# Kernel tuning notes

Hardware: AMD Instinct MI355X
Metric: run time of the kernel (lower is better)

The kernel has to match this reference:

```python
import jax, jax.numpy as jnp
import numpy as np

N_NODES = 50000
N_EDGES = 640000
WIDTH = 128
K = 5
N_CONVS = 6  # 1 input + 4 hidden + 1 output ChebConv layers


def setup_inputs() -> dict:
    key = jax.random.key(0)
    k1, k2, k3, k4 = jax.random.split(key, 4)
    scale = 1.0 / np.sqrt(WIDTH)
    x = jax.random.normal(k1, (N_NODES, WIDTH), dtype=jnp.float32)
    edge_index = jax.random.randint(k2, (2, N_EDGES), 0, N_NODES, dtype=jnp.int64)
    conv_w = jax.random.normal(k3, (N_CONVS, K, WIDTH, WIDTH), dtype=jnp.float32) * scale
    conv_b = jnp.zeros((N_CONVS, WIDTH), dtype=jnp.float32)
    lin_w = jax.random.normal(k4, (WIDTH, 1), dtype=jnp.float32) * scale
    lin_b = jnp.zeros((1,), dtype=jnp.float32)
    return {"x": x, "edge_index": edge_index, "conv_w": conv_w,
            "conv_b": conv_b, "lin_w": lin_w, "lin_b": lin_b}


def _cheb_norm(edge_index):
    # PyG ChebConv with normalization='sym', lambda_max=2.0:
    # L_hat = 2/lambda_max * (I - D^-1/2 A D^-1/2) - I = -D^-1/2 A D^-1/2
    # (diagonal terms cancel), so per-edge weight = -d_i^-1/2 * d_j^-1/2.
    src, dst = edge_index[0], edge_index[1]
    ones = jnp.ones((edge_index.shape[1],), dtype=jnp.float32)
    deg = jax.ops.segment_sum(ones, dst, num_segments=N_NODES)
    d_inv_sqrt = jnp.where(deg > 0, jax.lax.rsqrt(jnp.maximum(deg, 1e-12)), 0.0)
    return -d_inv_sqrt[src] * d_inv_sqrt[dst]


def _propagate(x, src, dst, norm):
    # L_hat @ x via gather -> weight -> scatter-add
    msg = norm[:, None] * x[src]              # [E, C]
    return jax.ops.segment_sum(msg, dst, num_segments=N_NODES)


def _cheb_conv(x, W, b, src, dst, norm):
    # Chebyshev recurrence: T0=x, T1=Lx, Tk = 2*L*T(k-1) - T(k-2)
    Tx0 = x
    out = Tx0 @ W[0]
    Tx1 = _propagate(Tx0, src, dst, norm)
    out = out + Tx1 @ W[1]
    for k in range(2, K):
        Tx2 = 2.0 * _propagate(Tx1, src, dst, norm) - Tx0
        out = out + Tx2 @ W[k]
        Tx0, Tx1 = Tx1, Tx2
    return out + b


def reference(x, edge_index, conv_w, conv_b, lin_w, lin_b):
    src, dst = edge_index[0], edge_index[1]
    norm = _cheb_norm(edge_index)
    h = x
    # first 5 convs followed by ReLU (dropout is identity in eval mode)
    for l in range(N_CONVS - 1):
        h = _cheb_conv(h, conv_w[l], conv_b[l], src, dst, norm)
        h = jax.nn.relu(h)
    # final conv (no activation) + Linear(128, 1)
    h = _cheb_conv(h, conv_w[N_CONVS - 1], conv_b[N_CONVS - 1], src, dst, norm)
    return h @ lin_w + lin_b
```

## Files before the change

kernel.cpp:

```cpp
#include <hip/hip_runtime.h>


#define NN 50000
#define NE 640000
#define WID 128
#define PROP_BLOCKS 2048

typedef __attribute__((ext_vector_type(8))) short bf16x8;
typedef __attribute__((ext_vector_type(4))) float f32x4;

__device__ __forceinline__ unsigned short f2bf(float f) {
  union { float f; unsigned int u; } v; v.f = f;
  unsigned int r = v.u + 0x7FFF + ((v.u >> 16) & 1);
  return (unsigned short)(r >> 16);
}
__device__ __forceinline__ unsigned int pack2(float lo, float hi) {
  return (unsigned int)f2bf(lo) | ((unsigned int)f2bf(hi) << 16);
}
__device__ __forceinline__ float bflo(unsigned int u) {
  return __uint_as_float(u << 16);
}
__device__ __forceinline__ float bfhi(unsigned int u) {
  return __uint_as_float(u & 0xffff0000u);
}
__device__ __forceinline__ float dec_norm(unsigned int p) {
  unsigned int lo = p & 0xfffu;
  float v = -__uint_as_float(((112u + ((p >> 8) & 15u)) << 23) | ((p & 255u) << 15));
  return (lo == 0u) ? 0.f : v;
}


__global__ __launch_bounds__(256) void degree_kernel(const int* __restrict__ ei,
                                                     int* __restrict__ deg, int E) {
  int e = blockIdx.x * 256 + threadIdx.x;
  if (e < E) atomicAdd(&deg[ei[E + e]], 1);
}

__global__ __launch_bounds__(256) void scan1_kernel(const int* __restrict__ deg,
                                                    int* __restrict__ lex,
                                                    int* __restrict__ bsum,
                                                    float* __restrict__ dinv, int n) {
  __shared__ int ws[4];
  int tid = threadIdx.x, lane = tid & 63, w = tid >> 6;
  int i = blockIdx.x * 256 + tid;
  int cnt = (i < n) ? deg[i] : 0;
  if (i < n) {
    float d = (float)cnt;
    dinv[i] = d > 0.0f ? rsqrtf(d) : 0.0f;
  }
  int v = cnt;
#pragma unroll
  for (int off = 1; off < 64; off <<= 1) {
    int u = __shfl_up(v, off, 64);
    if (lane >= off) v += u;
  }
  if (lane == 63) ws[w] = v;
  __syncthreads();
  int wexcl = 0;
#pragma unroll
  for (int k = 0; k < 4; ++k) wexcl += (k < w) ? ws[k] : 0;
  if (i < n) lex[i] = wexcl + v - cnt;
  if (tid == 255) bsum[blockIdx.x] = wexcl + v;
}

__global__ __launch_bounds__(256) void scan2_kernel(const int* __restrict__ bsum,
                                                    int* __restrict__ boff,
                                                    int* __restrict__ row_end, int nb) {
  __shared__ int ws[4];
  int tid = threadIdx.x, lane = tid & 63, w = tid >> 6;
  int cnt = (tid < nb) ? bsum[tid] : 0;
  int v = cnt;
#pragma unroll
  for (int off = 1; off < 64; off <<= 1) {
    int u = __shfl_up(v, off, 64);
    if (lane >= off) v += u;
  }
  if (lane == 63) ws[w] = v;
  __syncthreads();
  int wexcl = 0;
#pragma unroll
  for (int k = 0; k < 4; ++k) wexcl += (k < w) ? ws[k] : 0;
  if (tid < nb) boff[tid] = wexcl + v - cnt;
  if (tid == 255) *row_end = wexcl + v;
}

__global__ __launch_bounds__(256) void scan3_kernel(const int* __restrict__ lex,
                                                    const int* __restrict__ boff,
                                                    int* __restrict__ row_start,
                                                    int* __restrict__ fill_ptr, int n) {
  int i = blockIdx.x * 256 + threadIdx.x;
  if (i < n) {
    int rs = lex[i] + boff[blockIdx.x];
    row_start[i] = rs;
    fill_ptr[i] = rs;
  }
}

__global__ __launch_bounds__(256) void fill_kernel(const int* __restrict__ ei,
                                                   const float* __restrict__ dinv,
                                                   int* __restrict__ fill_ptr,
                                                   unsigned int* __restrict__ csr, int E) {
  int e = blockIdx.x * 256 + threadIdx.x;
  if (e < E) {
    int s = ei[e];
    int d = ei[E + e];
    int pos = atomicAdd(&fill_ptr[d], 1);
    float mag = dinv[s] * dinv[d];
    unsigned int bits = __float_as_uint(mag);
    unsigned int pk = (unsigned int)s << 12;
    if (bits != 0u) {
      bits += 0x4000u;
      int ex = (int)((bits >> 23) & 255u) - 112;
      ex = max(0, min(15, ex));
      pk |= ((unsigned int)ex << 8) | ((bits >> 15) & 0xffu);
    }
    csr[pos] = pk;
  }
}

__global__ __launch_bounds__(256) void cvt_kernel(const float* __restrict__ x,
                                                  unsigned short* __restrict__ xo,
                                                  const float* __restrict__ w,
                                                  unsigned short* __restrict__ wt,
                                                  int nx, int nw) {
  int i = blockIdx.x * 256 + threadIdx.x;
  if (i < nx) {
    xo[i] = f2bf(x[i]);
  } else if (i < nx + nw) {
    int j = i - nx;
    int l = j / (WID * 640);
    int r = j % (WID * 640);
    int col = r / 640;
    int k = r % 640;
    int kk = k >> 7, m = k & 127;
    wt[j] = f2bf(w[(((size_t)l * 5 + kk) * WID + m) * WID + col]);
  }
}

__global__ __launch_bounds__(256) void vk_kernel(const float* __restrict__ w,
                                                 const float* __restrict__ b,
                                                 const float* __restrict__ lw,
                                                 const float* __restrict__ lb,
                                                 float* __restrict__ V,
                                                 float* __restrict__ cst) {
  int tid = threadIdx.x;
  for (int idx = tid; idx < 5 * WID; idx += 256) {
    int k = idx / WID, i = idx % WID;
    const float* wr = w + (((size_t)5 * 5 + k) * WID + i) * WID;
    float s = 0.f;
#pragma unroll 4
    for (int j = 0; j < WID; ++j) s += wr[j] * lw[j];
    V[idx] = s;
  }
  if (tid == 0) {
    float s = 0.f;
    for (int c = 0; c < WID; ++c) s += b[5 * WID + c] * lw[c];
    *cst = s + lb[0];
  }
}


__global__ __launch_bounds__(256) void prop_kernel(unsigned short* __restrict__ out,
                                                   const unsigned short* __restrict__ xin,
                                                   const unsigned short* __restrict__ sub,
                                                   float scale,
                                                   const int* __restrict__ row_start,
                                                   const unsigned int* __restrict__ csr,
                                                   int n) {
  int t = threadIdx.x & 15;
  for (int node = blockIdx.x * 16 + (threadIdx.x >> 4); node < n;
       node += PROP_BLOCKS * 16) {
    int s = row_start[node], e = row_start[node + 1];
    float a0 = 0.f, a1 = 0.f, a2 = 0.f, a3 = 0.f;
    float a4 = 0.f, a5 = 0.f, a6 = 0.f, a7 = 0.f;
    for (int base = s; base < e; base += 16) {
      int cnt = min(16, e - base);
      unsigned int ed = (t < cnt) ? csr[base + t] : 0u;
      int j = 0;
      for (; j + 4 <= cnt; j += 4) {
        unsigned int p0 = (unsigned int)__shfl((int)ed, j, 16);
        unsigned int p1 = (unsigned int)__shfl((int)ed, j + 1, 16);
        unsigned int p2 = (unsigned int)__shfl((int)ed, j + 2, 16);
        unsigned int p3 = (unsigned int)__shfl((int)ed, j + 3, 16);
        int s0 = p0 >> 12, s1 = p1 >> 12, s2 = p2 >> 12, s3 = p3 >> 12;
        float n0 = dec_norm(p0), n1 = dec_norm(p1), n2 = dec_norm(p2), n3 = dec_norm(p3);
        const uint4 v0 = *(const uint4*)(xin + (size_t)s0 * WID + t * 8);
        const uint4 v1 = *(const uint4*)(xin + (size_t)s1 * WID + t * 8);
        const uint4 v2 = *(const uint4*)(xin + (size_t)s2 * WID + t * 8);
        const uint4 v3 = *(const uint4*)(xin + (size_t)s3 * WID + t * 8);
        a0 += n0 * bflo(v0.x) + n1 * bflo(v1.x) + n2 * bflo(v2.x) + n3 * bflo(v3.x);
        a1 += n0 * bfhi(v0.x) + n1 * bfhi(v1.x) + n2 * bfhi(v2.x) + n3 * bfhi(v3.x);
        a2 += n0 * bflo(v0.y) + n1 * bflo(v1.y) + n2 * bflo(v2.y) + n3 * bflo(v3.y);
        a3 += n0 * bfhi(v0.y) + n1 * bfhi(v1.y) + n2 * bfhi(v2.y) + n3 * bfhi(v3.y);
        a4 += n0 * bflo(v0.z) + n1 * bflo(v1.z) + n2 * bflo(v2.z) + n3 * bflo(v3.z);
        a5 += n0 * bfhi(v0.z) + n1 * bfhi(v1.z) + n2 * bfhi(v2.z) + n3 * bfhi(v3.z);
        a6 += n0 * bflo(v0.w) + n1 * bflo(v1.w) + n2 * bflo(v2.w) + n3 * bflo(v3.w);
        a7 += n0 * bfhi(v0.w) + n1 * bfhi(v1.w) + n2 * bfhi(v2.w) + n3 * bfhi(v3.w);
      }
      for (; j < cnt; ++j) {
        unsigned int pj = (unsigned int)__shfl((int)ed, j, 16);
        int sj = pj >> 12;
        float nj = dec_norm(pj);
        const uint4 v = *(const uint4*)(xin + (size_t)sj * WID + t * 8);
        a0 += nj * bflo(v.x); a1 += nj * bfhi(v.x);
        a2 += nj * bflo(v.y); a3 += nj * bfhi(v.y);
        a4 += nj * bflo(v.z); a5 += nj * bfhi(v.z);
        a6 += nj * bflo(v.w); a7 += nj * bfhi(v.w);
      }
    }
    size_t o = (size_t)node * WID + t * 8;
    float r0 = scale * a0, r1 = scale * a1, r2 = scale * a2, r3 = scale * a3;
    float r4 = scale * a4, r5 = scale * a5, r6 = scale * a6, r7 = scale * a7;
    if (sub) {
      const uint4 sv = *(const uint4*)(sub + o);
      r0 -= bflo(sv.x); r1 -= bfhi(sv.x);
      r2 -= bflo(sv.y); r3 -= bfhi(sv.y);
      r4 -= bflo(sv.z); r5 -= bfhi(sv.z);
      r6 -= bflo(sv.w); r7 -= bfhi(sv.w);
    }
    uint4 wv;
    wv.x = pack2(r0, r1); wv.y = pack2(r2, r3);
    wv.z = pack2(r4, r5); wv.w = pack2(r6, r7);
    *(uint4*)(out + o) = wv;
  }
}

__global__ __launch_bounds__(256) void final_proj(const unsigned short* __restrict__ H,
                                                  const float* __restrict__ V,
                                                  const float* __restrict__ cstp,
                                                  float* __restrict__ U,
                                                  float* __restrict__ y, int n) {
  int t = threadIdx.x & 15;
  int node = blockIdx.x * 16 + (threadIdx.x >> 4);
  if (node >= n) return;
  const uint4 h = *(const uint4*)(H + (size_t)node * WID + t * 8);
  float hv0 = bflo(h.x), hv1 = bfhi(h.x), hv2 = bflo(h.y), hv3 = bfhi(h.y);
  float hv4 = bflo(h.z), hv5 = bfhi(h.z), hv6 = bflo(h.w), hv7 = bfhi(h.w);
  float p[5];
#pragma unroll
  for (int k = 0; k < 5; ++k) {
    const float4* vp = (const float4*)(V + k * WID + t * 8);
    float4 v0 = vp[0], v1 = vp[1];
    float s = hv0 * v0.x + hv1 * v0.y + hv2 * v0.z + hv3 * v0.w +
              hv4 * v1.x + hv5 * v1.y + hv6 * v1.z + hv7 * v1.w;
#pragma unroll
    for (int off = 1; off < 16; off <<= 1) s += __shfl_xor(s, off, 16);
    p[k] = s;
  }
  if (t == 0) {
    float4 u0 = {p[0], p[1], p[2], p[3]};
    float4 u1 = {p[4], 0.f, 0.f, 0.f};
    *(float4*)(U + (size_t)node * 8) = u0;
    *(float4*)(U + (size_t)node * 8 + 4) = u1;
    y[node] = p[0] + *cstp;
  }
}

__global__ __launch_bounds__(256) void prop_small(float* __restrict__ out,
                                                  const float* __restrict__ xin,
                                                  const float* __restrict__ sub,
                                                  float scale, int pick,
                                                  float* __restrict__ y,
                                                  const int* __restrict__ row_start,
                                                  const unsigned int* __restrict__ csr,
                                                  int n) {
  int node = blockIdx.x * 256 + threadIdx.x;
  if (node >= n) return;
  int s = row_start[node], e = row_start[node + 1];
  float a0 = 0.f, a1 = 0.f, a2 = 0.f, a3 = 0.f;
  float a4 = 0.f, a5 = 0.f, a6 = 0.f, a7 = 0.f;
  for (int i = s; i < e; ++i) {
    unsigned int p = csr[i];
    int src = (int)(p >> 12);
    float nv = dec_norm(p);
    const float4* r = (const float4*)(xin + (size_t)src * 8);
    float4 v0 = r[0], v1 = r[1];
    a0 += nv * v0.x; a1 += nv * v0.y; a2 += nv * v0.z; a3 += nv * v0.w;
    a4 += nv * v1.x; a5 += nv * v1.y; a6 += nv * v1.z; a7 += nv * v1.w;
  }
  float o0 = scale * a0, o1 = scale * a1, o2 = scale * a2, o3 = scale * a3;
  float o4 = scale * a4, o5 = scale * a5, o6 = scale * a6, o7 = scale * a7;
  if (sub) {
    const float4* sv = (const float4*)(sub + (size_t)node * 8);
    float4 s0 = sv[0], s1 = sv[1];
    o0 -= s0.x; o1 -= s0.y; o2 -= s0.z; o3 -= s0.w;
    o4 -= s1.x; o5 -= s1.y; o6 -= s1.z; o7 -= s1.w;
  }
  float4 w0 = {o0, o1, o2, o3};
  float4 w1 = {o4, o5, o6, o7};
  *(float4*)(out + (size_t)node * 8) = w0;
  *(float4*)(out + (size_t)node * 8 + 4) = w1;
  float yp = o1;
  if (pick == 2) yp = o2;
  if (pick == 3) yp = o3;
  if (pick == 4) yp = o4;
  y[node] += yp;
}


__global__ __launch_bounds__(256) void cheb_gemm(
    const unsigned short* __restrict__ T0, const unsigned short* __restrict__ T1,
    const unsigned short* __restrict__ T2, const unsigned short* __restrict__ T3,
    const unsigned short* __restrict__ T4,
    const unsigned short* __restrict__ Wt,
    const float* __restrict__ bias,
    unsigned short* __restrict__ Hb, int M) {
  __shared__ unsigned short As[64][72];
  __shared__ unsigned short Bs[128][72];
  const unsigned short* chunks[5] = {T0, T1, T2, T3, T4};
  int tid = threadIdx.x;
  int wave = tid >> 6, lane = tid & 63;
  int lrow = lane & 15, quad = lane >> 4;
  int rowBase = blockIdx.x * 64;

  f32x4 acc[8];
#pragma unroll
  for (int b = 0; b < 8; ++b) acc[b] = (f32x4){0.f, 0.f, 0.f, 0.f};

  int ar = tid >> 2, aseg = (tid & 3) * 16;
  int agrow = min(rowBase + ar, M - 1);
  int bc = tid >> 1, bseg = (tid & 1) * 32;

  int4 aR0, aR1, bR0, bR1, bR2, bR3;
  {
    const unsigned short* ap = chunks[0] + (size_t)agrow * WID + aseg;
    aR0 = *(const int4*)ap;
    aR1 = *(const int4*)(ap + 8);
    const unsigned short* bp = Wt + (size_t)bc * 640 + bseg;
    bR0 = *(const int4*)bp;
    bR1 = *(const int4*)(bp + 8);
    bR2 = *(const int4*)(bp + 16);
    bR3 = *(const int4*)(bp + 24);
  }

  for (int kc = 0; kc < 10; ++kc) {
    *(int4*)(&As[ar][aseg]) = aR0;
    *(int4*)(&As[ar][aseg + 8]) = aR1;
    *(int4*)(&Bs[bc][bseg]) = bR0;
    *(int4*)(&Bs[bc][bseg + 8]) = bR1;
    *(int4*)(&Bs[bc][bseg + 16]) = bR2;
    *(int4*)(&Bs[bc][bseg + 24]) = bR3;
    __syncthreads();

    if (kc < 9) {
      int kn = kc + 1;
      const unsigned short* ap =
          chunks[kn >> 1] + (size_t)agrow * WID + (kn & 1) * 64 + aseg;
      aR0 = *(const int4*)ap;
      aR1 = *(const int4*)(ap + 8);
      const unsigned short* bp = Wt + (size_t)bc * 640 + kn * 64 + bseg;
      bR0 = *(const int4*)bp;
      bR1 = *(const int4*)(bp + 8);
      bR2 = *(const int4*)(bp + 16);
      bR3 = *(const int4*)(bp + 24);
    }

    bf16x8 a0 = *(bf16x8*)(&As[wave * 16 + lrow][quad * 8]);
    bf16x8 a1 = *(bf16x8*)(&As[wave * 16 + lrow][32 + quad * 8]);
#pragma unroll
    for (int ct = 0; ct < 8; ++ct) {
      bf16x8 b0 = *(bf16x8*)(&Bs[ct * 16 + lrow][quad * 8]);
      acc[ct] = __builtin_amdgcn_mfma_f32_16x16x32_bf16(a0, b0, acc[ct], 0, 0, 0);
      bf16x8 b1 = *(bf16x8*)(&Bs[ct * 16 + lrow][32 + quad * 8]);
      acc[ct] = __builtin_amdgcn_mfma_f32_16x16x32_bf16(a1, b1, acc[ct], 0, 0, 0);
    }
    __syncthreads();
  }

#pragma unroll
  for (int ct = 0; ct < 8; ++ct) {
    int gcol = ct * 16 + lrow;
    float bv = bias[gcol];
#pragma unroll
    for (int reg = 0; reg < 4; ++reg) {
      int grow = rowBase + wave * 16 + quad * 4 + reg;
      if (grow < M) {
        float v = fmaxf(acc[ct][reg] + bv, 0.f);
        Hb[(size_t)grow * WID + gcol] = f2bf(v);
      }
    }
  }
}


extern "C" void kernel_launch(void* const* d_in, const int* in_sizes, int n_in,
                              void* d_out, int out_size, void* d_ws, size_t ws_size,
                              hipStream_t stream) {
  const float* x = (const float*)d_in[0];
  const int* ei = (const int*)d_in[1];
  const float* conv_w = (const float*)d_in[2];
  const float* conv_b = (const float*)d_in[3];
  const float* lin_w = (const float*)d_in[4];
  const float* lin_b = (const float*)d_in[5];

  const int N = NN, E = NE, C = WID, L = 6;
  const int NB = (N + 255) / 256;

  char* ws = (char*)d_ws;
  size_t off = 0;
  auto alloc = [&](size_t bytes) -> void* {
    void* p = ws + off;
    off = (off + bytes + 255) & ~(size_t)255;
    return p;
  };
  int* deg = (int*)alloc((size_t)N * 4);
  float* dinv = (float*)alloc((size_t)N * 4);
  int* row_start = (int*)alloc((size_t)(N + 1) * 4);
  int* fill_ptr = (int*)alloc((size_t)N * 4);
  int* lex = (int*)alloc((size_t)N * 4);
  int* bsum = (int*)alloc((size_t)NB * 4);
  int* boff = (int*)alloc((size_t)NB * 4);
  unsigned int* csr = (unsigned int*)alloc((size_t)E * 4);
  unsigned short* Xbf = (unsigned short*)alloc((size_t)N * C * 2);
  unsigned short* Hb0 = (unsigned short*)alloc((size_t)N * C * 2);
  unsigned short* Hb1 = (unsigned short*)alloc((size_t)N * C * 2);
  unsigned short* T1b = (unsigned short*)alloc((size_t)N * C * 2);
  unsigned short* T2b = (unsigned short*)alloc((size_t)N * C * 2);
  unsigned short* T3b = (unsigned short*)alloc((size_t)N * C * 2);
  unsigned short* T4b = (unsigned short*)alloc((size_t)N * C * 2);
  unsigned short* Wt = (unsigned short*)alloc((size_t)5 * C * 640 * 2);
  float* V = (float*)alloc((size_t)5 * C * 4);
  float* cst = (float*)alloc(4);

  hipMemsetAsync(deg, 0, (size_t)N * 4, stream);
  degree_kernel<<<(E + 255) / 256, 256, 0, stream>>>(ei, deg, E);
  scan1_kernel<<<NB, 256, 0, stream>>>(deg, lex, bsum, dinv, N);
  scan2_kernel<<<1, 256, 0, stream>>>(bsum, boff, &row_start[N], NB);
  scan3_kernel<<<NB, 256, 0, stream>>>(lex, boff, row_start, fill_ptr, N);
  fill_kernel<<<(E + 255) / 256, 256, 0, stream>>>(ei, dinv, fill_ptr, csr, E);
  {
    int nx = N * C, nw = 5 * C * 640;
    cvt_kernel<<<(nx + nw + 255) / 256, 256, 0, stream>>>(x, Xbf, conv_w, Wt, nx, nw);
  }
  vk_kernel<<<1, 256, 0, stream>>>(conv_w, conv_b, lin_w, lin_b, V, cst);

  const int gg = (N + 63) / 64;

  for (int l = 0; l < 5; ++l) {
    const unsigned short* T0 = (l == 0) ? Xbf : ((l & 1) ? Hb0 : Hb1);
    unsigned short* Hb = (l & 1) ? Hb1 : Hb0;

    prop_kernel<<<PROP_BLOCKS, 256, 0, stream>>>(T1b, T0, nullptr, 1.0f, row_start, csr, N);
    prop_kernel<<<PROP_BLOCKS, 256, 0, stream>>>(T2b, T1b, T0, 2.0f, row_start, csr, N);
    prop_kernel<<<PROP_BLOCKS, 256, 0, stream>>>(T3b, T2b, T1b, 2.0f, row_start, csr, N);
    prop_kernel<<<PROP_BLOCKS, 256, 0, stream>>>(T4b, T3b, T2b, 2.0f, row_start, csr, N);
    cheb_gemm<<<gg, 256, 0, stream>>>(T0, T1b, T2b, T3b, T4b,
                                      Wt + (size_t)l * C * 640, conv_b + (size_t)l * C,
                                      Hb, N);
  }

  {
    float* y = (float*)d_out;
    float* U  = (float*)T1b;
    float* P1 = (float*)T2b;
    float* P2 = (float*)T3b;
    float* P3 = (float*)T4b;
    float* P4 = (float*)Xbf;
    const int pg = (N + 255) / 256;
    final_proj<<<(N + 15) / 16, 256, 0, stream>>>(Hb0, V, cst, U, y, N);
    prop_small<<<pg, 256, 0, stream>>>(P1, U, nullptr, 1.0f, 1, y, row_start, csr, N);
    prop_small<<<pg, 256, 0, stream>>>(P2, P1, U, 2.0f, 2, y, row_start, csr, N);
    prop_small<<<pg, 256, 0, stream>>>(P3, P2, P1, 2.0f, 3, y, row_start, csr, N);
    prop_small<<<pg, 256, 0, stream>>>(P4, P3, P2, 2.0f, 4, y, row_start, csr, N);
  }
}
```

Measured before the change: 859.0 us.

## Fuse final Chebyshev propagation into GEMM via shared-memory T4 tile

The fourth propagation step (T4 = 2*L*T3 - T2) now runs inside the GEMM kernel. Each block computes its 64 rows of T4 into shared memory and feeds them to the MFMA loop for the last two K-chunks, so the separate prop launch and the T4 global write and read-back go away. In exchange the GEMM blocks do irregular gather work before any MFMA, use more LDS (lower occupancy), and get less parallelism for the gather (782 blocks instead of 2048). The vk kernel is also spread over 3 blocks and vectorised with float4 loads.

```diff
diff --git a/kernel.cpp b/kernel.cpp
--- a/kernel.cpp
+++ b/kernel.cpp
@@ -143,16 +143,20 @@
                                                  const float* __restrict__ lb,
                                                  float* __restrict__ V,
                                                  float* __restrict__ cst) {
-  int tid = threadIdx.x;
-  for (int idx = tid; idx < 5 * WID; idx += 256) {
+  int idx = blockIdx.x * 256 + threadIdx.x;
+  if (idx < 5 * WID) {
     int k = idx / WID, i = idx % WID;
-    const float* wr = w + (((size_t)5 * 5 + k) * WID + i) * WID;
+    const float4* wr = (const float4*)(w + (((size_t)5 * 5 + k) * WID + i) * WID);
+    const float4* l4 = (const float4*)lw;
     float s = 0.f;
-#pragma unroll 4
-    for (int j = 0; j < WID; ++j) s += wr[j] * lw[j];
+#pragma unroll 8
+    for (int j = 0; j < WID / 4; ++j) {
+      float4 a = wr[j], c = l4[j];
+      s += a.x * c.x + a.y * c.y + a.z * c.z + a.w * c.w;
+    }
     V[idx] = s;
   }
-  if (tid == 0) {
+  if (blockIdx.x == 0 && threadIdx.x == 0) {
     float s = 0.f;
     for (int c = 0; c < WID; ++c) s += b[5 * WID + c] * lw[c];
     *cst = s + lb[0];
@@ -298,20 +302,83 @@
 }
 
 
-__global__ __launch_bounds__(256) void cheb_gemm(
+__global__ __launch_bounds__(256) void cheb_gemm_fused(
     const unsigned short* __restrict__ T0, const unsigned short* __restrict__ T1,
     const unsigned short* __restrict__ T2, const unsigned short* __restrict__ T3,
-    const unsigned short* __restrict__ T4,
     const unsigned short* __restrict__ Wt,
     const float* __restrict__ bias,
+    const int* __restrict__ row_start,
+    const unsigned int* __restrict__ csr,
     unsigned short* __restrict__ Hb, int M) {
   __shared__ unsigned short As[64][72];
   __shared__ unsigned short Bs[128][72];
-  const unsigned short* chunks[5] = {T0, T1, T2, T3, T4};
+  __shared__ unsigned short T4s[64][136];
+  const unsigned short* chunks[4] = {T0, T1, T2, T3};
   int tid = threadIdx.x;
   int wave = tid >> 6, lane = tid & 63;
   int lrow = lane & 15, quad = lane >> 4;
   int rowBase = blockIdx.x * 64;
+
+  {
+    int t = tid & 15;
+    int slot = tid >> 4;
+#pragma unroll
+    for (int round = 0; round < 4; ++round) {
+      int r = round * 16 + slot;
+      int node = rowBase + r;
+      if (node < M) {
+        int s = row_start[node], e = row_start[node + 1];
+        float a0 = 0.f, a1 = 0.f, a2 = 0.f, a3 = 0.f;
+        float a4 = 0.f, a5 = 0.f, a6 = 0.f, a7 = 0.f;
+        for (int base = s; base < e; base += 16) {
+          int cnt = min(16, e - base);
+          unsigned int ed = (t < cnt) ? csr[base + t] : 0u;
+          int j = 0;
+          for (; j + 4 <= cnt; j += 4) {
+            unsigned int p0 = (unsigned int)__shfl((int)ed, j, 16);
+            unsigned int p1 = (unsigned int)__shfl((int)ed, j + 1, 16);
+            unsigned int p2 = (unsigned int)__shfl((int)ed, j + 2, 16);
+            unsigned int p3 = (unsigned int)__shfl((int)ed, j + 3, 16);
+            int s0 = p0 >> 12, s1 = p1 >> 12, s2 = p2 >> 12, s3 = p3 >> 12;
+            float n0 = dec_norm(p0), n1 = dec_norm(p1);
+            float n2 = dec_norm(p2), n3 = dec_norm(p3);
+            const uint4 v0 = *(const uint4*)(T3 + (size_t)s0 * WID + t * 8);
+            const uint4 v1 = *(const uint4*)(T3 + (size_t)s1 * WID + t * 8);
+            const uint4 v2 = *(const uint4*)(T3 + (size_t)s2 * WID + t * 8);
+            const uint4 v3 = *(const uint4*)(T3 + (size_t)s3 * WID + t * 8);
+            a0 += n0 * bflo(v0.x) + n1 * bflo(v1.x) + n2 * bflo(v2.x) + n3 * bflo(v3.x);
+            a1 += n0 * bfhi(v0.x) + n1 * bfhi(v1.x) + n2 * bfhi(v2.x) + n3 * bfhi(v3.x);
+            a2 += n0 * bflo(v0.y) + n1 * bflo(v1.y) + n2 * bflo(v2.y) + n3 * bflo(v3.y);
+            a3 += n0 * bfhi(v0.y) + n1 * bfhi(v1.y) + n2 * bfhi(v2.y) + n3 * bfhi(v3.y);
+            a4 += n0 * bflo(v0.z) + n1 * bflo(v1.z) + n2 * bflo(v2.z) + n3 * bflo(v3.z);
+            a5 += n0 * bfhi(v0.z) + n1 * bfhi(v1.z) + n2 * bfhi(v2.z) + n3 * bfhi(v3.z);
+            a6 += n0 * bflo(v0.w) + n1 * bflo(v1.w) + n2 * bflo(v2.w) + n3 * bflo(v3.w);
+            a7 += n0 * bfhi(v0.w) + n1 * bfhi(v1.w) + n2 * bfhi(v2.w) + n3 * bfhi(v3.w);
+          }
+          for (; j < cnt; ++j) {
+            unsigned int pj = (unsigned int)__shfl((int)ed, j, 16);
+            int sj = pj >> 12;
+            float nj = dec_norm(pj);
+            const uint4 v = *(const uint4*)(T3 + (size_t)sj * WID + t * 8);
+            a0 += nj * bflo(v.x); a1 += nj * bfhi(v.x);
+            a2 += nj * bflo(v.y); a3 += nj * bfhi(v.y);
+            a4 += nj * bflo(v.z); a5 += nj * bfhi(v.z);
+            a6 += nj * bflo(v.w); a7 += nj * bfhi(v.w);
+          }
+        }
+        const uint4 sv = *(const uint4*)(T2 + (size_t)node * WID + t * 8);
+        float r0 = 2.f * a0 - bflo(sv.x), r1 = 2.f * a1 - bfhi(sv.x);
+        float r2 = 2.f * a2 - bflo(sv.y), r3 = 2.f * a3 - bfhi(sv.y);
+        float r4 = 2.f * a4 - bflo(sv.z), r5 = 2.f * a5 - bfhi(sv.z);
+        float r6 = 2.f * a6 - bflo(sv.w), r7 = 2.f * a7 - bfhi(sv.w);
+        uint4 wv;
+        wv.x = pack2(r0, r1); wv.y = pack2(r2, r3);
+        wv.z = pack2(r4, r5); wv.w = pack2(r6, r7);
+        *(uint4*)(&T4s[r][t * 8]) = wv;
+      }
+    }
+  }
+  __syncthreads();
 
   f32x4 acc[8];
 #pragma unroll
@@ -334,8 +401,10 @@
   }
 
   for (int kc = 0; kc < 10; ++kc) {
-    *(int4*)(&As[ar][aseg]) = aR0;
-    *(int4*)(&As[ar][aseg + 8]) = aR1;
+    if (kc < 8) {
+      *(int4*)(&As[ar][aseg]) = aR0;
+      *(int4*)(&As[ar][aseg + 8]) = aR1;
+    }
     *(int4*)(&Bs[bc][bseg]) = bR0;
     *(int4*)(&Bs[bc][bseg + 8]) = bR1;
     *(int4*)(&Bs[bc][bseg + 16]) = bR2;
@@ -344,10 +413,12 @@
 
     if (kc < 9) {
       int kn = kc + 1;
-      const unsigned short* ap =
-          chunks[kn >> 1] + (size_t)agrow * WID + (kn & 1) * 64 + aseg;
-      aR0 = *(const int4*)ap;
-      aR1 = *(const int4*)(ap + 8);
+      if (kn < 8) {
+        const unsigned short* ap =
+            chunks[kn >> 1] + (size_t)agrow * WID + (kn & 1) * 64 + aseg;
+        aR0 = *(const int4*)ap;
+        aR1 = *(const int4*)(ap + 8);
+      }
       const unsigned short* bp = Wt + (size_t)bc * 640 + kn * 64 + bseg;
       bR0 = *(const int4*)bp;
       bR1 = *(const int4*)(bp + 8);
@@ -355,8 +426,15 @@
       bR3 = *(const int4*)(bp + 24);
     }
 
-    bf16x8 a0 = *(bf16x8*)(&As[wave * 16 + lrow][quad * 8]);
-    bf16x8 a1 = *(bf16x8*)(&As[wave * 16 + lrow][32 + quad * 8]);
+    bf16x8 a0, a1;
+    if (kc < 8) {
+      a0 = *(bf16x8*)(&As[wave * 16 + lrow][quad * 8]);
+      a1 = *(bf16x8*)(&As[wave * 16 + lrow][32 + quad * 8]);
+    } else {
+      int ko = (kc - 8) * 64;
+      a0 = *(bf16x8*)(&T4s[wave * 16 + lrow][ko + quad * 8]);
+      a1 = *(bf16x8*)(&T4s[wave * 16 + lrow][ko + 32 + quad * 8]);
+    }
 #pragma unroll
     for (int ct = 0; ct < 8; ++ct) {
       bf16x8 b0 = *(bf16x8*)(&Bs[ct * 16 + lrow][quad * 8]);
@@ -432,7 +510,7 @@
     int nx = N * C, nw = 5 * C * 640;
     cvt_kernel<<<(nx + nw + 255) / 256, 256, 0, stream>>>(x, Xbf, conv_w, Wt, nx, nw);
   }
-  vk_kernel<<<1, 256, 0, stream>>>(conv_w, conv_b, lin_w, lin_b, V, cst);
+  vk_kernel<<<3, 256, 0, stream>>>(conv_w, conv_b, lin_w, lin_b, V, cst);
 
   const int gg = (N + 63) / 64;
 
@@ -443,10 +521,10 @@
     prop_kernel<<<PROP_BLOCKS, 256, 0, stream>>>(T1b, T0, nullptr, 1.0f, row_start, csr, N);
     prop_kernel<<<PROP_BLOCKS, 256, 0, stream>>>(T2b, T1b, T0, 2.0f, row_start, csr, N);
     prop_kernel<<<PROP_BLOCKS, 256, 0, stream>>>(T3b, T2b, T1b, 2.0f, row_start, csr, N);
-    prop_kernel<<<PROP_BLOCKS, 256, 0, stream>>>(T4b, T3b, T2b, 2.0f, row_start, csr, N);
-    cheb_gemm<<<gg, 256, 0, stream>>>(T0, T1b, T2b, T3b, T4b,
-                                      Wt + (size_t)l * C * 640, conv_b + (size_t)l * C,
-                                      Hb, N);
+    cheb_gemm_fused<<<gg, 256, 0, stream>>>(T0, T1b, T2b, T3b,
+                                            Wt + (size_t)l * C * 640,
+                                            conv_b + (size_t)l * C,
+                                            row_start, csr, Hb, N);
   }
 
   {
```

Measured after the change: 937.1 us. 1.09x slower.
